# Optimization experiments

Hardware: AMD Instinct MI355X
Metric: run time of the kernel (lower is better)

The kernel has to match this reference:

```python
import jax, jax.numpy as jnp
import numpy as np

D_MODEL = 768
N_HEADS = 12
D_HEAD = D_MODEL // N_HEADS
TEMP = float(np.sqrt(D_HEAD))


def setup_inputs() -> dict:
    key = jax.random.key(0)
    ks = jax.random.split(key, 12)
    B, S, D = 8, 2048, D_MODEL
    patches = jax.random.normal(ks[0], (B, S, D), dtype=jnp.float32)
    in_weight = jax.random.uniform(ks[1], (D * 3, D), dtype=jnp.float32)
    in_bias = jax.random.uniform(ks[2], (D * 3,), dtype=jnp.float32)
    out_w = jax.random.normal(ks[3], (D, D), dtype=jnp.float32) * (1.0 / np.sqrt(D))
    out_b = jnp.zeros((D,), dtype=jnp.float32)
    mlp_w1 = jax.random.normal(ks[4], (4 * D, D), dtype=jnp.float32) * (1.0 / np.sqrt(D))
    mlp_b1 = jnp.zeros((4 * D,), dtype=jnp.float32)
    mlp_w2 = jax.random.normal(ks[5], (D, 4 * D), dtype=jnp.float32) * (1.0 / np.sqrt(4 * D))
    mlp_b2 = jnp.zeros((D,), dtype=jnp.float32)
    ln1_g = jnp.ones((D,), dtype=jnp.float32)
    ln1_b = jnp.zeros((D,), dtype=jnp.float32)
    ln2_g = jnp.ones((D,), dtype=jnp.float32)
    ln2_b = jnp.zeros((D,), dtype=jnp.float32)
    return {
        "patches": patches,
        "in_weight": in_weight, "in_bias": in_bias,
        "out_w": out_w, "out_b": out_b,
        "mlp_w1": mlp_w1, "mlp_b1": mlp_b1,
        "mlp_w2": mlp_w2, "mlp_b2": mlp_b2,
        "ln1_g": ln1_g, "ln1_b": ln1_b,
        "ln2_g": ln2_g, "ln2_b": ln2_b,
    }


def layer_norm(x, g, b, eps=1e-5):
    mu = jnp.mean(x, axis=-1, keepdims=True)
    var = jnp.var(x, axis=-1, keepdims=True)
    return (x - mu) * jax.lax.rsqrt(var + eps) * g + b


def mha(x, in_weight, in_bias, out_w, out_b):
    # Replicate quirky per-head reshape: [3D, D] -> [H, d_head, 3, D]
    W = in_weight.reshape(N_HEADS, D_HEAD, 3, D_MODEL)  # h, e, 3, d
    Bv = in_bias.reshape(N_HEADS, D_HEAD, 3)            # h, e, 3
    qw, kw, vw = W[:, :, 0, :], W[:, :, 1, :], W[:, :, 2, :]  # [H, e, D]
    qb, kb, vb = Bv[:, :, 0], Bv[:, :, 1], Bv[:, :, 2]        # [H, e]
    # Q,K,V per head: [B, H, S, e]
    Q = jnp.einsum('bsd,hed->bhse', x, qw) + qb[None, :, None, :]
    K = jnp.einsum('bsd,hed->bhse', x, kw) + kb[None, :, None, :]
    V = jnp.einsum('bsd,hed->bhse', x, vw) + vb[None, :, None, :]
    atn = jnp.einsum('bhse,bhte->bhst', Q, K)
    atn = jax.nn.softmax(atn / TEMP, axis=-1)
    # NOTE: original uses V (not atn @ V) as head output; heads concatenated over feature dim
    B_, H, S, e = V.shape
    heads = jnp.transpose(V, (0, 2, 1, 3)).reshape(B_, S, H * e)
    masks = jnp.sum(atn, axis=1)  # sum over heads: [B, S, S]
    out = heads @ out_w.T + out_b
    return out, masks


def reference(patches, in_weight, in_bias, out_w, out_b,
              mlp_w1, mlp_b1, mlp_w2, mlp_b2,
              ln1_g, ln1_b, ln2_g, ln2_b):
    x = layer_norm(patches, ln1_g, ln1_b)
    sa, _ = mha(x, in_weight, in_bias, out_w, out_b)
    x = sa + x  # dropout = identity (eval)
    x = layer_norm(x, ln2_g, ln2_b)
    h = jax.nn.selu(x @ mlp_w1.T + mlp_b1)
    x = (h @ mlp_w2.T + mlp_b2) + x
    return x
```

## Files before the change

kernel.cpp:

```cpp
#include <hip/hip_runtime.h>


typedef __bf16 bf16;
typedef __bf16 bf16x8 __attribute__((ext_vector_type(8)));
typedef __bf16 bf16x4 __attribute__((ext_vector_type(4)));
typedef float  f32x4  __attribute__((ext_vector_type(4)));

#define N_ROWS  16384

#define AS1(p) ((const __attribute__((address_space(1))) void*)(p))
#define AS3(p) ((__attribute__((address_space(3))) void*)(p))

__global__ __launch_bounds__(256) void cast_kernel(const float* __restrict__ x,
                                                   bf16* __restrict__ y, int n4) {
  int i = blockIdx.x * 256 + threadIdx.x;
  if (i >= n4) return;
  float4 v = ((const float4*)x)[i];
  bf16x4 o = {(bf16)v.x, (bf16)v.y, (bf16)v.z, (bf16)v.w};
  *(bf16x4*)(y + 4 * (size_t)i) = o;
}

__global__ __launch_bounds__(256) void wvt_kernel(const float* __restrict__ in_weight,
                                                  bf16* __restrict__ wvt) {
  int k = blockIdx.x * 256 + threadIdx.x;
  int j = blockIdx.y;
  wvt[(size_t)k * 768 + j] = (bf16)in_weight[((size_t)j * 3 + 2) * 768 + k];
}

__global__ __launch_bounds__(64) void bias_combine_kernel(const float* __restrict__ out_w,
                                                          const float* __restrict__ in_bias,
                                                          const float* __restrict__ out_b,
                                                          float* __restrict__ bc) {
  int n = blockIdx.x, l = threadIdx.x;
  float s = 0.f;
  for (int j = l; j < 768; j += 64) s += out_w[(size_t)n * 768 + j] * in_bias[j * 3 + 2];
#pragma unroll
  for (int off = 32; off > 0; off >>= 1) s += __shfl_xor(s, off, 64);
  if (l == 0) bc[n] = s + out_b[n];
}

__global__ __launch_bounds__(256) void ln_kernel(const float* __restrict__ x,
                                                 const float* __restrict__ g,
                                                 const float* __restrict__ b,
                                                 bf16* __restrict__ y) {
  const int row = blockIdx.x;
  const float* xr = x + (size_t)row * 768;
  float v[3], s1 = 0.f, s2 = 0.f;
#pragma unroll
  for (int i = 0; i < 3; ++i) {
    v[i] = xr[threadIdx.x + i * 256];
    s1 += v[i];
    s2 += v[i] * v[i];
  }
#pragma unroll
  for (int off = 32; off > 0; off >>= 1) {
    s1 += __shfl_xor(s1, off, 64);
    s2 += __shfl_xor(s2, off, 64);
  }
  __shared__ float red[8];
  int w = threadIdx.x >> 6, l = threadIdx.x & 63;
  if (l == 0) { red[w * 2] = s1; red[w * 2 + 1] = s2; }
  __syncthreads();
  s1 = red[0] + red[2] + red[4] + red[6];
  s2 = red[1] + red[3] + red[5] + red[7];
  const float mu = s1 * (1.f / 768.f);
  const float var = s2 * (1.f / 768.f) - mu * mu;
  const float rstd = rsqrtf(var + 1e-5f);
#pragma unroll
  for (int i = 0; i < 3; ++i) {
    int d = threadIdx.x + i * 256;
    y[(size_t)row * 768 + d] = (bf16)((v[i] - mu) * rstd * g[d] + b[d]);
  }
}

template <int EPI>
__global__ __launch_bounds__(256, 2) void gemm_bt(const bf16* __restrict__ A,
                                                  const bf16* __restrict__ B,
                                                  const float* __restrict__ bias,
                                                  const bf16* __restrict__ resid,
                                                  void* __restrict__ out,
                                                  int M, int N, int K) {
  __shared__ bf16 sA0[128 * 32], sA1[128 * 32];
  __shared__ bf16 sB0[256 * 32], sB1[256 * 32];
  const int tid = threadIdx.x;
  const int w = tid >> 6, l = tid & 63;
  const int q = l >> 4, m16 = l & 15;

  int mtile, ntile;
  {
    const int L = blockIdx.y * gridDim.x + blockIdx.x;
    const int gy = gridDim.y;
    if ((gy & 7) == 0) {
      const int mpx = gy >> 3;
      const int xcd = L & 7;
      const int slot = L >> 3;
      mtile = xcd * mpx + (slot % mpx);
      ntile = slot / mpx;
    } else {
      mtile = blockIdx.y; ntile = blockIdx.x;
    }
  }
  const long tileM = (long)mtile * 128;
  const long tileN = (long)ntile * 256;

  const bf16* gA[2]; int ldA[2];
#pragma unroll
  for (int i = 0; i < 2; ++i) {
    const int ch = tid + i * 256;
    const int row = ch >> 2;
    const int cl = ((ch & 3) - (row >> 1)) & 3;
    gA[i] = A + (tileM + row) * (long)K + cl * 8;
    ldA[i] = ch * 8;
  }
  const bf16* gB[4]; int ldB[4];
#pragma unroll
  for (int j = 0; j < 4; ++j) {
    const int ch = tid + j * 256;
    const int row = ch >> 2;
    const int cl = ((ch & 3) - (row >> 1)) & 3;
    gB[j] = B + (tileN + row) * (long)K + cl * 8;
    ldB[j] = ch * 8;
  }

  int offA[8], offB[4];
#pragma unroll
  for (int mi = 0; mi < 8; ++mi) {
    const int r = mi * 16 + m16;
    offA[mi] = r * 32 + (((q + (r >> 1)) & 3) << 3);
  }
#pragma unroll
  for (int ni = 0; ni < 4; ++ni) {
    const int r = w * 64 + ni * 16 + m16;
    offB[ni] = r * 32 + (((q + (r >> 1)) & 3) << 3);
  }

  f32x4 acc[8][4] = {};

#pragma unroll
  for (int i = 0; i < 2; ++i)
    __builtin_amdgcn_global_load_lds(AS1(gA[i]), AS3(&sA0[ldA[i]]), 16, 0, 0);
#pragma unroll
  for (int j = 0; j < 4; ++j)
    __builtin_amdgcn_global_load_lds(AS1(gB[j]), AS3(&sB0[ldB[j]]), 16, 0, 0);
  __syncthreads();

  const bf16 *cra = sA0, *crb = sB0;
  bf16 *nxa = sA1, *nxb = sB1;

  for (long k0 = 32; k0 < K; k0 += 32) {
#pragma unroll
    for (int i = 0; i < 2; ++i)
      __builtin_amdgcn_global_load_lds(AS1(gA[i] + k0), AS3(&nxa[ldA[i]]), 16, 0, 0);
#pragma unroll
    for (int j = 0; j < 4; ++j)
      __builtin_amdgcn_global_load_lds(AS1(gB[j] + k0), AS3(&nxb[ldB[j]]), 16, 0, 0);

    bf16x8 bfr[4];
#pragma unroll
    for (int ni = 0; ni < 4; ++ni) bfr[ni] = *(const bf16x8*)&crb[offB[ni]];
#pragma unroll
    for (int mi = 0; mi < 8; ++mi) {
      const bf16x8 af = *(const bf16x8*)&cra[offA[mi]];
#pragma unroll
      for (int ni = 0; ni < 4; ++ni)
        acc[mi][ni] = __builtin_amdgcn_mfma_f32_16x16x32_bf16(af, bfr[ni],
                                                              acc[mi][ni], 0, 0, 0);
    }

    __syncthreads();

    const bf16* ta = cra; cra = nxa; nxa = (bf16*)ta;
    const bf16* tb = crb; crb = nxb; nxb = (bf16*)tb;
  }

  {
    bf16x8 bfr[4];
#pragma unroll
    for (int ni = 0; ni < 4; ++ni) bfr[ni] = *(const bf16x8*)&crb[offB[ni]];
#pragma unroll
    for (int mi = 0; mi < 8; ++mi) {
      const bf16x8 af = *(const bf16x8*)&cra[offA[mi]];
#pragma unroll
      for (int ni = 0; ni < 4; ++ni)
        acc[mi][ni] = __builtin_amdgcn_mfma_f32_16x16x32_bf16(af, bfr[ni],
                                                              acc[mi][ni], 0, 0, 0);
    }
  }

  const long colBase = tileN + (long)w * 64 + m16;
  const long rowBase = tileM + q * 4;
#pragma unroll
  for (int mi = 0; mi < 8; ++mi) {
#pragma unroll
    for (int r = 0; r < 4; ++r) {
      const long row = rowBase + mi * 16 + r;
#pragma unroll
      for (int ni = 0; ni < 4; ++ni) {
        const long col = colBase + ni * 16;
        float v = acc[mi][ni][r];
        if (EPI == 0) {
          ((bf16*)out)[row * N + col] = (bf16)v;
        } else if (EPI == 1) {
          v += bias[col] + (float)resid[row * N + col];
          ((float*)out)[row * N + col] = v;
        } else {
          v += bias[col];
          v = v > 0.f ? 1.0507009873554805f * v
                      : 1.0507009873554805f * 1.6732632423543772f * (__expf(v) - 1.f);
          ((bf16*)out)[row * N + col] = (bf16)v;
        }
      }
    }
  }
}

extern "C" void kernel_launch(void* const* d_in, const int* in_sizes, int n_in,
                              void* d_out, int out_size, void* d_ws, size_t ws_size,
                              hipStream_t stream) {
  const float* patches   = (const float*)d_in[0];
  const float* in_weight = (const float*)d_in[1];
  const float* in_bias   = (const float*)d_in[2];
  const float* out_w     = (const float*)d_in[3];
  const float* out_b     = (const float*)d_in[4];
  const float* mlp_w1    = (const float*)d_in[5];
  const float* mlp_b1    = (const float*)d_in[6];
  const float* mlp_w2    = (const float*)d_in[7];
  const float* mlp_b2    = (const float*)d_in[8];
  const float* ln1_g     = (const float*)d_in[9];
  const float* ln1_b     = (const float*)d_in[10];
  const float* ln2_g     = (const float*)d_in[11];
  const float* ln2_b     = (const float*)d_in[12];

  char* ws = (char*)d_ws;
  const size_t MB = 1024 * 1024;
  bf16* Wc   = (bf16*)(ws + 0);
  bf16* w1b  = (bf16*)(ws + 2 * MB);
  bf16* w2b  = (bf16*)(ws + 8 * MB);
  bf16* owb  = (bf16*)(ws + 14 * MB);
  bf16* wvt  = (bf16*)(ws + 16 * MB);
  float* bc  = (float*)(ws + 18 * MB);
  bf16* X1   = (bf16*)(ws + 20 * MB);
  bf16* X3   = (bf16*)(ws + 20 * MB);
  bf16* H    = (bf16*)(ws + 48 * MB);
  float* X2  = (float*)d_out;

  cast_kernel<<<(3072 * 768 / 4 + 255) / 256, 256, 0, stream>>>(mlp_w1, w1b, 3072 * 768 / 4);
  cast_kernel<<<(768 * 3072 / 4 + 255) / 256, 256, 0, stream>>>(mlp_w2, w2b, 768 * 3072 / 4);
  cast_kernel<<<(768 * 768 / 4 + 255) / 256, 256, 0, stream>>>(out_w, owb, 768 * 768 / 4);
  wvt_kernel<<<dim3(3, 768), 256, 0, stream>>>(in_weight, wvt);
  bias_combine_kernel<<<768, 64, 0, stream>>>(out_w, in_bias, out_b, bc);
  gemm_bt<0><<<dim3(3, 6), 256, 0, stream>>>(owb, wvt, nullptr, nullptr, Wc, 768, 768, 768);

  ln_kernel<<<N_ROWS, 256, 0, stream>>>(patches, ln1_g, ln1_b, X1);
  gemm_bt<1><<<dim3(3, 128), 256, 0, stream>>>(X1, Wc, bc, X1, X2, N_ROWS, 768, 768);
  ln_kernel<<<N_ROWS, 256, 0, stream>>>(X2, ln2_g, ln2_b, X3);
  gemm_bt<2><<<dim3(12, 128), 256, 0, stream>>>(X3, w1b, mlp_b1, nullptr, H, N_ROWS, 3072, 768);
  gemm_bt<1><<<dim3(3, 128), 256, 0, stream>>>(H, w2b, mlp_b2, X3, d_out, N_ROWS, 768, 3072);
}
```

Before: 409.2 us.

## Triple-buffer GEMM LDS tiles with explicit vmcnt waits and one barrier per step

Replaces the double-buffered shared-memory A/B tiles in the bf16 GEMM with a three-slot ring. Prefetch now runs two K-steps ahead, issued after a partial vmcnt wait and a single barrier per step. The main loop is unrolled by three so slot indices are compile-time constants. The goal is to hide global-to-LDS load latency behind MFMA work and drop the trailing __syncthreads per iteration. The cost is 50% more LDS per block, which can limit occupancy, and the code assumes K/32 is a multiple of three.

```diff
diff --git a/kernel.cpp b/kernel.cpp
--- a/kernel.cpp
+++ b/kernel.cpp
@@ -10,6 +10,9 @@
 
 #define AS1(p) ((const __attribute__((address_space(1))) void*)(p))
 #define AS3(p) ((__attribute__((address_space(3))) void*)(p))
+
+#define WAIT_VM6 0x0F76
+#define WAIT_VM0 0x0F70
 
 __global__ __launch_bounds__(256) void cast_kernel(const float* __restrict__ x,
                                                    bf16* __restrict__ y, int n4) {
@@ -73,6 +76,44 @@
   }
 }
 
+#define SLOT_ELEMS (384 * 32)
+
+template <int SLOT, int WIMM>
+__device__ __forceinline__ void kstep(bf16* __restrict__ ring,
+                                      const bf16* const (&gA)[2],
+                                      const bf16* const (&gB)[4],
+                                      const int (&ldA)[2], const int (&ldB)[4],
+                                      const int (&offA)[8], const int (&offB)[4],
+                                      f32x4 (&acc)[8][4], long& k_next,
+                                      bool doIssue) {
+  __builtin_amdgcn_s_waitcnt(WIMM);
+  __builtin_amdgcn_s_barrier();
+  if (doIssue) {
+    bf16* da = ring + ((SLOT + 2) % 3) * SLOT_ELEMS;
+    bf16* db = da + 128 * 32;
+#pragma unroll
+    for (int i = 0; i < 2; ++i)
+      __builtin_amdgcn_global_load_lds(AS1(gA[i] + k_next), AS3(&da[ldA[i]]), 16, 0, 0);
+#pragma unroll
+    for (int j = 0; j < 4; ++j)
+      __builtin_amdgcn_global_load_lds(AS1(gB[j] + k_next), AS3(&db[ldB[j]]), 16, 0, 0);
+    k_next += 32;
+  }
+  const bf16* ca = ring + SLOT * SLOT_ELEMS;
+  const bf16* cb = ca + 128 * 32;
+  bf16x8 bfr[4];
+#pragma unroll
+  for (int ni = 0; ni < 4; ++ni) bfr[ni] = *(const bf16x8*)&cb[offB[ni]];
+#pragma unroll
+  for (int mi = 0; mi < 8; ++mi) {
+    const bf16x8 af = *(const bf16x8*)&ca[offA[mi]];
+#pragma unroll
+    for (int ni = 0; ni < 4; ++ni)
+      acc[mi][ni] = __builtin_amdgcn_mfma_f32_16x16x32_bf16(af, bfr[ni],
+                                                            acc[mi][ni], 0, 0, 0);
+  }
+}
+
 template <int EPI>
 __global__ __launch_bounds__(256, 2) void gemm_bt(const bf16* __restrict__ A,
                                                   const bf16* __restrict__ B,
@@ -80,8 +121,7 @@
                                                   const bf16* __restrict__ resid,
                                                   void* __restrict__ out,
                                                   int M, int N, int K) {
-  __shared__ bf16 sA0[128 * 32], sA1[128 * 32];
-  __shared__ bf16 sB0[256 * 32], sB1[256 * 32];
+  __shared__ bf16 ring[3 * SLOT_ELEMS];
   const int tid = threadIdx.x;
   const int w = tid >> 6, l = tid & 63;
   const int q = l >> 4, m16 = l & 15;
@@ -137,55 +177,28 @@
   f32x4 acc[8][4] = {};
 
 #pragma unroll
-  for (int i = 0; i < 2; ++i)
-    __builtin_amdgcn_global_load_lds(AS1(gA[i]), AS3(&sA0[ldA[i]]), 16, 0, 0);
-#pragma unroll
-  for (int j = 0; j < 4; ++j)
-    __builtin_amdgcn_global_load_lds(AS1(gB[j]), AS3(&sB0[ldB[j]]), 16, 0, 0);
-  __syncthreads();
-
-  const bf16 *cra = sA0, *crb = sB0;
-  bf16 *nxa = sA1, *nxb = sB1;
-
-  for (long k0 = 32; k0 < K; k0 += 32) {
+  for (int s = 0; s < 2; ++s) {
+    bf16* da = ring + s * SLOT_ELEMS;
+    bf16* db = da + 128 * 32;
 #pragma unroll
     for (int i = 0; i < 2; ++i)
-      __builtin_amdgcn_global_load_lds(AS1(gA[i] + k0), AS3(&nxa[ldA[i]]), 16, 0, 0);
+      __builtin_amdgcn_global_load_lds(AS1(gA[i] + s * 32), AS3(&da[ldA[i]]), 16, 0, 0);
 #pragma unroll
     for (int j = 0; j < 4; ++j)
-      __builtin_amdgcn_global_load_lds(AS1(gB[j] + k0), AS3(&nxb[ldB[j]]), 16, 0, 0);
-
-    bf16x8 bfr[4];
-#pragma unroll
-    for (int ni = 0; ni < 4; ++ni) bfr[ni] = *(const bf16x8*)&crb[offB[ni]];
-#pragma unroll
-    for (int mi = 0; mi < 8; ++mi) {
-      const bf16x8 af = *(const bf16x8*)&cra[offA[mi]];
-#pragma unroll
-      for (int ni = 0; ni < 4; ++ni)
-        acc[mi][ni] = __builtin_amdgcn_mfma_f32_16x16x32_bf16(af, bfr[ni],
-                                                              acc[mi][ni], 0, 0, 0);
-    }
-
-    __syncthreads();
-
-    const bf16* ta = cra; cra = nxa; nxa = (bf16*)ta;
-    const bf16* tb = crb; crb = nxb; nxb = (bf16*)tb;
-  }
-
-  {
-    bf16x8 bfr[4];
-#pragma unroll
-    for (int ni = 0; ni < 4; ++ni) bfr[ni] = *(const bf16x8*)&crb[offB[ni]];
-#pragma unroll
-    for (int mi = 0; mi < 8; ++mi) {
-      const bf16x8 af = *(const bf16x8*)&cra[offA[mi]];
-#pragma unroll
-      for (int ni = 0; ni < 4; ++ni)
-        acc[mi][ni] = __builtin_amdgcn_mfma_f32_16x16x32_bf16(af, bfr[ni],
-                                                              acc[mi][ni], 0, 0, 0);
-    }
-  }
+      __builtin_amdgcn_global_load_lds(AS1(gB[j] + s * 32), AS3(&db[ldB[j]]), 16, 0, 0);
+  }
+  long k_next = 64;
+
+  const int T = K >> 5;
+#pragma unroll 1
+  for (int g = 0; g < T - 3; g += 3) {
+    kstep<0, WAIT_VM6>(ring, gA, gB, ldA, ldB, offA, offB, acc, k_next, true);
+    kstep<1, WAIT_VM6>(ring, gA, gB, ldA, ldB, offA, offB, acc, k_next, true);
+    kstep<2, WAIT_VM6>(ring, gA, gB, ldA, ldB, offA, offB, acc, k_next, true);
+  }
+  kstep<0, WAIT_VM6>(ring, gA, gB, ldA, ldB, offA, offB, acc, k_next, true);
+  kstep<1, WAIT_VM6>(ring, gA, gB, ldA, ldB, offA, offB, acc, k_next, false);
+  kstep<2, WAIT_VM0>(ring, gA, gB, ldA, ldB, offA, offB, acc, k_next, false);
 
   const long colBase = tileN + (long)w * 64 + m16;
   const long rowBase = tileM + q * 4;
```

Result: no change. 413.6 us (+1.1%).
